# Optimization experiments

Measured on AMD Instinct MI355X. Metric: run time of the kernel, lower is better.

Reference implementation:

```python
import jax, jax.numpy as jnp
import numpy as np


def setup_inputs() -> dict:
    key = jax.random.key(0)
    k1, k2 = jax.random.split(key)
    B, Q = 256, 16
    ry_angles = jax.random.normal(k1, (B, Q), dtype=jnp.float32)
    rz_angles = jax.random.normal(k2, (B, Q), dtype=jnp.float32)
    return {"ry_angles": ry_angles, "rz_angles": rz_angles}


def reference(ry_angles, rz_angles):
    # Per-qubit composite gate rz*ry applied to |0>: only the first column matters.
    # entry11 = cos(ry/2) * exp(-i rz/2), entry21 = sin(ry/2) * exp(+i rz/2)
    half_ry = ry_angles * 0.5
    half_rz = rz_angles * 0.5
    c = jnp.cos(half_ry).astype(jnp.complex64)
    s = jnp.sin(half_ry).astype(jnp.complex64)
    e_neg = jnp.exp(-1j * half_rz.astype(jnp.complex64))
    e_pos = jnp.exp(1j * half_rz.astype(jnp.complex64))
    cols = jnp.stack([c * e_neg, s * e_pos], axis=-1)  # [B, Q, 2]
    B, Q = ry_angles.shape
    # State vector = Kronecker product over qubits (qubit 0 = most significant bit),
    # built iteratively: vector doubles in length each qubit.
    v = jnp.ones((B, 1), dtype=jnp.complex64)
    for q in range(Q):
        v = (v[:, :, None] * cols[:, q][:, None, :]).reshape(B, -1)
    return v  # [B, 2**Q] complex64
```

## Files before the change

kernel.cpp:

```cpp
#include <hip/hip_runtime.h>


typedef __attribute__((ext_vector_type(4))) float fvec4;

__device__ __forceinline__ float2 cmul(float2 a, float2 b) {
    return make_float2(fmaf(a.x, b.x, -a.y * b.y),
                       fmaf(a.x, b.y,  a.y * b.x));
}

__device__ __forceinline__ void build_AB(const float* __restrict__ ry,
                                         const float* __restrict__ rz,
                                         int b, int t,
                                         float2 (&cols)[16][2],
                                         float2 (&A)[256], float2 (&Bv)[256]) {
    if (t < 16) {
        float hry = 0.5f * ry[b * 16 + t];
        float hrz = 0.5f * rz[b * 16 + t];
        float s, c, sz, cz;
        sincosf(hry, &s, &c);
        sincosf(hrz, &sz, &cz);
        cols[t][0] = make_float2(c * cz, -c * sz);
        cols[t][1] = make_float2(s * cz,  s * sz);
    }
    __syncthreads();
    float2 a = cols[0][(t >> 7) & 1];
    #pragma unroll
    for (int q = 1; q < 8; ++q) a = cmul(a, cols[q][(t >> (7 - q)) & 1]);
    A[t] = a;
    float2 bv = cols[8][(t >> 7) & 1];
    #pragma unroll
    for (int q = 9; q < 16; ++q) bv = cmul(bv, cols[q][(t >> (15 - q)) & 1]);
    Bv[t] = bv;
    __syncthreads();
}

__global__ __launch_bounds__(256) void encoder_real_f32(
        const float* __restrict__ ry, const float* __restrict__ rz,
        fvec4* __restrict__ out) {
    __shared__ float2 cols[16][2];
    __shared__ float2 A[256];
    __shared__ float2 Bv[256];
    const int b = blockIdx.x, slice = blockIdx.y, t = threadIdx.x;
    build_AB(ry, rz, b, t, cols, A, Bv);

    const int jp = t & 63;
    const int wv = t >> 6;
    const float2 b0 = Bv[4 * jp + 0], b1 = Bv[4 * jp + 1];
    const float2 b2 = Bv[4 * jp + 2], b3 = Bv[4 * jp + 3];

    const int row0 = slice * 16 + wv * 4;
    const float2 a0 = A[row0 + 0];
    const float2 a1 = A[row0 + 1];
    const float2 a2 = A[row0 + 2];
    const float2 a3 = A[row0 + 3];

    fvec4* outb = out + (size_t)b * 16384 + (size_t)row0 * 64 + jp;
    fvec4 w0, w1, w2, w3;
    w0[0] = fmaf(a0.x, b0.x, -a0.y * b0.y);
    w0[1] = fmaf(a0.x, b1.x, -a0.y * b1.y);
    w0[2] = fmaf(a0.x, b2.x, -a0.y * b2.y);
    w0[3] = fmaf(a0.x, b3.x, -a0.y * b3.y);
    w1[0] = fmaf(a1.x, b0.x, -a1.y * b0.y);
    w1[1] = fmaf(a1.x, b1.x, -a1.y * b1.y);
    w1[2] = fmaf(a1.x, b2.x, -a1.y * b2.y);
    w1[3] = fmaf(a1.x, b3.x, -a1.y * b3.y);
    w2[0] = fmaf(a2.x, b0.x, -a2.y * b0.y);
    w2[1] = fmaf(a2.x, b1.x, -a2.y * b1.y);
    w2[2] = fmaf(a2.x, b2.x, -a2.y * b2.y);
    w2[3] = fmaf(a2.x, b3.x, -a2.y * b3.y);
    w3[0] = fmaf(a3.x, b0.x, -a3.y * b0.y);
    w3[1] = fmaf(a3.x, b1.x, -a3.y * b1.y);
    w3[2] = fmaf(a3.x, b2.x, -a3.y * b2.y);
    w3[3] = fmaf(a3.x, b3.x, -a3.y * b3.y);
    __builtin_nontemporal_store(w0, outb +   0);
    __builtin_nontemporal_store(w1, outb +  64);
    __builtin_nontemporal_store(w2, outb + 128);
    __builtin_nontemporal_store(w3, outb + 192);
}

__global__ __launch_bounds__(256) void encoder_ileave_f32(
        const float* __restrict__ ry, const float* __restrict__ rz,
        fvec4* __restrict__ out) {
    __shared__ float2 cols[16][2];
    __shared__ float2 A[256];
    __shared__ float2 Bv[256];
    const int b = blockIdx.x, slice = blockIdx.y, t = threadIdx.x;
    build_AB(ry, rz, b, t, cols, A, Bv);

    const int jp   = t & 127;
    const int half = t >> 7;
    const float2 b0 = Bv[2 * jp], b1 = Bv[2 * jp + 1];
    fvec4* outb = out + (size_t)b * 32768;
    const int row0 = slice * 64 + half * 32;
    #pragma unroll 4
    for (int i = row0; i < row0 + 32; ++i) {
        const float2 ai = A[i];
        const float2 r0 = cmul(ai, b0), r1 = cmul(ai, b1);
        fvec4 w; w[0] = r0.x; w[1] = r0.y; w[2] = r1.x; w[3] = r1.y;
        __builtin_nontemporal_store(w, &outb[(size_t)i * 128 + jp]);
    }
}

extern "C" void kernel_launch(void* const* d_in, const int* in_sizes, int n_in,
                              void* d_out, int out_size, void* d_ws, size_t ws_size,
                              hipStream_t stream) {
    const float* ry = (const float*)d_in[0];
    const float* rz = (const float*)d_in[1];

    const int B = in_sizes[0] / 16;
    const long long pairs = (long long)B << 16;
    dim3 block(256, 1, 1);
    if ((long long)out_size >= 2 * pairs) {
        dim3 grid(B, 4, 1);
        encoder_ileave_f32<<<grid, block, 0, stream>>>(ry, rz, (fvec4*)d_out);
    } else {
        dim3 grid(B, 16, 1);
        encoder_real_f32<<<grid, block, 0, stream>>>(ry, rz, (fvec4*)d_out);
    }
}
```

Measured before the change: 78.44 us.

## Split table construction into a separate kernel and stream outer product from workspace

Moves the per-batch A/B half-state table computation into a dedicated kernel that writes to workspace, so the output kernels no longer recompute sincos and chained complex products per block. The streaming kernels load the tables from global memory with vector loads and skip shared memory and barriers. This removes redundant work across the slices of each batch but adds a second kernel launch and a global round trip for the tables.

```diff
diff --git a/kernel.cpp b/kernel.cpp
--- a/kernel.cpp
+++ b/kernel.cpp
@@ -8,11 +8,11 @@
                        fmaf(a.x, b.y,  a.y * b.x));
 }
 
-__device__ __forceinline__ void build_AB(const float* __restrict__ ry,
-                                         const float* __restrict__ rz,
-                                         int b, int t,
-                                         float2 (&cols)[16][2],
-                                         float2 (&A)[256], float2 (&Bv)[256]) {
+__global__ __launch_bounds__(256) void build_tables(
+        const float* __restrict__ ry, const float* __restrict__ rz,
+        float2* __restrict__ wsA, float2* __restrict__ wsB) {
+    __shared__ float2 cols[16][2];
+    const int b = blockIdx.x, t = threadIdx.x;
     if (t < 16) {
         float hry = 0.5f * ry[b * 16 + t];
         float hrz = 0.5f * rz[b * 16 + t];
@@ -26,75 +26,65 @@
     float2 a = cols[0][(t >> 7) & 1];
     #pragma unroll
     for (int q = 1; q < 8; ++q) a = cmul(a, cols[q][(t >> (7 - q)) & 1]);
-    A[t] = a;
+    wsA[b * 256 + t] = a;
     float2 bv = cols[8][(t >> 7) & 1];
     #pragma unroll
     for (int q = 9; q < 16; ++q) bv = cmul(bv, cols[q][(t >> (15 - q)) & 1]);
-    Bv[t] = bv;
-    __syncthreads();
+    wsB[b * 256 + t] = bv;
 }
 
-__global__ __launch_bounds__(256) void encoder_real_f32(
-        const float* __restrict__ ry, const float* __restrict__ rz,
+__global__ __launch_bounds__(256) void stream_outer(
+        const float2* __restrict__ wsA, const float2* __restrict__ wsB,
         fvec4* __restrict__ out) {
-    __shared__ float2 cols[16][2];
-    __shared__ float2 A[256];
-    __shared__ float2 Bv[256];
     const int b = blockIdx.x, slice = blockIdx.y, t = threadIdx.x;
-    build_AB(ry, rz, b, t, cols, A, Bv);
-
     const int jp = t & 63;
     const int wv = t >> 6;
-    const float2 b0 = Bv[4 * jp + 0], b1 = Bv[4 * jp + 1];
-    const float2 b2 = Bv[4 * jp + 2], b3 = Bv[4 * jp + 3];
+    const int row0 = slice * 16 + wv * 4;
 
-    const int row0 = slice * 16 + wv * 4;
-    const float2 a0 = A[row0 + 0];
-    const float2 a1 = A[row0 + 1];
-    const float2 a2 = A[row0 + 2];
-    const float2 a3 = A[row0 + 3];
+    const fvec4* bt = (const fvec4*)(wsB + b * 256) + 2 * jp;
+    const fvec4 bl0 = bt[0];
+    const fvec4 bl1 = bt[1];
+    const float2* at = wsA + b * 256 + row0;
+    const float2 a0 = at[0], a1 = at[1], a2 = at[2], a3 = at[3];
 
     fvec4* outb = out + (size_t)b * 16384 + (size_t)row0 * 64 + jp;
     fvec4 w0, w1, w2, w3;
-    w0[0] = fmaf(a0.x, b0.x, -a0.y * b0.y);
-    w0[1] = fmaf(a0.x, b1.x, -a0.y * b1.y);
-    w0[2] = fmaf(a0.x, b2.x, -a0.y * b2.y);
-    w0[3] = fmaf(a0.x, b3.x, -a0.y * b3.y);
-    w1[0] = fmaf(a1.x, b0.x, -a1.y * b0.y);
-    w1[1] = fmaf(a1.x, b1.x, -a1.y * b1.y);
-    w1[2] = fmaf(a1.x, b2.x, -a1.y * b2.y);
-    w1[3] = fmaf(a1.x, b3.x, -a1.y * b3.y);
-    w2[0] = fmaf(a2.x, b0.x, -a2.y * b0.y);
-    w2[1] = fmaf(a2.x, b1.x, -a2.y * b1.y);
-    w2[2] = fmaf(a2.x, b2.x, -a2.y * b2.y);
-    w2[3] = fmaf(a2.x, b3.x, -a2.y * b3.y);
-    w3[0] = fmaf(a3.x, b0.x, -a3.y * b0.y);
-    w3[1] = fmaf(a3.x, b1.x, -a3.y * b1.y);
-    w3[2] = fmaf(a3.x, b2.x, -a3.y * b2.y);
-    w3[3] = fmaf(a3.x, b3.x, -a3.y * b3.y);
+    w0[0] = fmaf(a0.x, bl0[0], -a0.y * bl0[1]);
+    w0[1] = fmaf(a0.x, bl0[2], -a0.y * bl0[3]);
+    w0[2] = fmaf(a0.x, bl1[0], -a0.y * bl1[1]);
+    w0[3] = fmaf(a0.x, bl1[2], -a0.y * bl1[3]);
+    w1[0] = fmaf(a1.x, bl0[0], -a1.y * bl0[1]);
+    w1[1] = fmaf(a1.x, bl0[2], -a1.y * bl0[3]);
+    w1[2] = fmaf(a1.x, bl1[0], -a1.y * bl1[1]);
+    w1[3] = fmaf(a1.x, bl1[2], -a1.y * bl1[3]);
+    w2[0] = fmaf(a2.x, bl0[0], -a2.y * bl0[1]);
+    w2[1] = fmaf(a2.x, bl0[2], -a2.y * bl0[3]);
+    w2[2] = fmaf(a2.x, bl1[0], -a2.y * bl1[1]);
+    w2[3] = fmaf(a2.x, bl1[2], -a2.y * bl1[3]);
+    w3[0] = fmaf(a3.x, bl0[0], -a3.y * bl0[1]);
+    w3[1] = fmaf(a3.x, bl0[2], -a3.y * bl0[3]);
+    w3[2] = fmaf(a3.x, bl1[0], -a3.y * bl1[1]);
+    w3[3] = fmaf(a3.x, bl1[2], -a3.y * bl1[3]);
     __builtin_nontemporal_store(w0, outb +   0);
     __builtin_nontemporal_store(w1, outb +  64);
     __builtin_nontemporal_store(w2, outb + 128);
     __builtin_nontemporal_store(w3, outb + 192);
 }
 
-__global__ __launch_bounds__(256) void encoder_ileave_f32(
-        const float* __restrict__ ry, const float* __restrict__ rz,
+__global__ __launch_bounds__(256) void stream_outer_ileave(
+        const float2* __restrict__ wsA, const float2* __restrict__ wsB,
         fvec4* __restrict__ out) {
-    __shared__ float2 cols[16][2];
-    __shared__ float2 A[256];
-    __shared__ float2 Bv[256];
     const int b = blockIdx.x, slice = blockIdx.y, t = threadIdx.x;
-    build_AB(ry, rz, b, t, cols, A, Bv);
-
-    const int jp   = t & 127;
+    const int jp = t & 127;
     const int half = t >> 7;
-    const float2 b0 = Bv[2 * jp], b1 = Bv[2 * jp + 1];
+    const fvec4 bl = ((const fvec4*)(wsB + b * 256))[jp];
+    const float2 b0 = make_float2(bl[0], bl[1]);
+    const float2 b1 = make_float2(bl[2], bl[3]);
     fvec4* outb = out + (size_t)b * 32768;
     const int row0 = slice * 64 + half * 32;
     #pragma unroll 4
     for (int i = row0; i < row0 + 32; ++i) {
-        const float2 ai = A[i];
+        const float2 ai = wsA[b * 256 + i];
         const float2 r0 = cmul(ai, b0), r1 = cmul(ai, b1);
         fvec4 w; w[0] = r0.x; w[1] = r0.y; w[2] = r1.x; w[3] = r1.y;
         __builtin_nontemporal_store(w, &outb[(size_t)i * 128 + jp]);
@@ -109,12 +99,14 @@
 
     const int B = in_sizes[0] / 16;
     const long long pairs = (long long)B << 16;
+    float2* wsA = (float2*)d_ws;
+    float2* wsB = wsA + (size_t)B * 256;
     dim3 block(256, 1, 1);
+
+    build_tables<<<dim3(B, 1, 1), block, 0, stream>>>(ry, rz, wsA, wsB);
     if ((long long)out_size >= 2 * pairs) {
-        dim3 grid(B, 4, 1);
-        encoder_ileave_f32<<<grid, block, 0, stream>>>(ry, rz, (fvec4*)d_out);
+        stream_outer_ileave<<<dim3(B, 4, 1), block, 0, stream>>>(wsA, wsB, (fvec4*)d_out);
     } else {
-        dim3 grid(B, 16, 1);
-        encoder_real_f32<<<grid, block, 0, stream>>>(ry, rz, (fvec4*)d_out);
+        stream_outer<<<dim3(B, 16, 1), block, 0, stream>>>(wsA, wsB, (fvec4*)d_out);
     }
 }
```

After: 81.39 us. 3.8% more time.
